# Kernel optimization log

Measured on AMD Instinct MI355X. Metric: run time of the kernel, lower is better.

Reference implementation:

```python
import jax, jax.numpy as jnp
import numpy as np

EMBED_DIM = 768
NUM_HEADS = 12
HEAD_DIM = EMBED_DIM // NUM_HEADS  # 64
SCALE = HEAD_DIM ** 0.5  # NOTE: source MULTIPLIES by sqrt(head_dim) (likely a bug, kept faithful)


def setup_inputs() -> dict:
    key = jax.random.key(0)
    kx, kq, kk, kv, ko = jax.random.split(key, 5)
    B, N, E = 8, 2048, EMBED_DIM
    s = 1.0 / np.sqrt(E)
    return {
        "x": jax.random.normal(kx, (B, N, E), dtype=jnp.float32),
        # nn.Linear weights stored [out_features, in_features], y = x @ W.T
        "Wq": jax.random.normal(kq, (E, E), dtype=jnp.float32) * s,
        "Wk": jax.random.normal(kk, (E, E), dtype=jnp.float32) * s,
        "Wv": jax.random.normal(kv, (E, E), dtype=jnp.float32) * s,
        "Wo": jax.random.normal(ko, (E, E), dtype=jnp.float32) * s,
    }


def reference(x, Wq, Wk, Wv, Wo):
    # Projections (no bias)
    q = jnp.einsum("bne,fe->bnf", x, Wq)
    k = jnp.einsum("bne,fe->bnf", x, Wk)
    v = jnp.einsum("bne,fe->bnf", x, Wv)
    # Full-width attention over the entire embedding dim (no head split, per source)
    energy = jnp.einsum("bid,bjd->bij", q, k) * SCALE  # [B, N, N]
    attn = jax.nn.softmax(energy, axis=-1)
    out = jnp.einsum("bij,bjd->bid", attn, v)  # [B, N, E]
    return jnp.einsum("bne,fe->bnf", out, Wo)
```

## Files before the change

### kernel.cpp

```cpp
#include <hip/hip_runtime.h>
#include <stdint.h>

typedef __bf16 bf16;
typedef __bf16 bf16x4 __attribute__((ext_vector_type(4)));
typedef __bf16 bf16x8 __attribute__((ext_vector_type(8)));
typedef float  f32x4  __attribute__((ext_vector_type(4)));

constexpr int BB = 8;
constexpr int NN = 2048;
constexpr int EE = 768;
constexpr int MM = BB * NN;
constexpr int E2 = 2 * EE;

typedef const __attribute__((address_space(1))) void* as1_cvp;
typedef __attribute__((address_space(3))) void* as3_vp;

static __device__ __forceinline__ void gld16(const void* g, void* l) {
  __builtin_amdgcn_global_load_lds((as1_cvp)g, (as3_vp)l, 16, 0, 0);
}

__global__ __launch_bounds__(256) void k_splitx(const float4* __restrict__ x,
                                                bf16x4* __restrict__ hi,
                                                bf16x4* __restrict__ lo, int n4) {
  int i = blockIdx.x * 256 + threadIdx.x;
  int st = gridDim.x * 256;
  for (; i < n4; i += st) {
    float4 v = x[i];
    bf16x4 h, l;
    h[0] = (bf16)v.x; l[0] = (bf16)(v.x - (float)h[0]);
    h[1] = (bf16)v.y; l[1] = (bf16)(v.y - (float)h[1]);
    h[2] = (bf16)v.z; l[2] = (bf16)(v.z - (float)h[2]);
    h[3] = (bf16)v.w; l[3] = (bf16)(v.w - (float)h[3]);
    hi[i] = h; lo[i] = l;
  }
}

__global__ __launch_bounds__(256) void k_wprep(const float4* __restrict__ wq,
                                               const float4* __restrict__ wk,
                                               const float4* __restrict__ wv,
                                               const float4* __restrict__ wo,
                                               bf16x4* __restrict__ qkh, bf16x4* __restrict__ qkl,
                                               bf16x4* __restrict__ vb,  bf16x4* __restrict__ ob) {
  const int n4 = EE * EE / 4;
  int sel = blockIdx.y;
  int i = blockIdx.x * 256 + threadIdx.x;
  int st = gridDim.x * 256;
  for (; i < n4; i += st) {
    if (sel <= 1) {
      float4 v = sel == 0 ? wq[i] : wk[i];
      bf16x4 h, l;
      h[0] = (bf16)v.x; l[0] = (bf16)(v.x - (float)h[0]);
      h[1] = (bf16)v.y; l[1] = (bf16)(v.y - (float)h[1]);
      h[2] = (bf16)v.z; l[2] = (bf16)(v.z - (float)h[2]);
      h[3] = (bf16)v.w; l[3] = (bf16)(v.w - (float)h[3]);
      int o = i + sel * n4;
      qkh[o] = h; qkl[o] = l;
    } else {
      float4 v = sel == 2 ? wv[i] : wo[i];
      bf16x4 h;
      h[0] = (bf16)v.x; h[1] = (bf16)v.y; h[2] = (bf16)v.z; h[3] = (bf16)v.w;
      if (sel == 2) vb[i] = h; else ob[i] = h;
    }
  }
}

template <bool SPLIT, int EPI>
__global__ __launch_bounds__(256, 2) void k_gemm(
    const bf16* __restrict__ Ah, const bf16* __restrict__ Al,
    const bf16* __restrict__ Bh, const bf16* __restrict__ Bl,
    void* __restrict__ C0, void* __restrict__ C1,
    int Kdim, int lda, int ldb, int ldc,
    long long sA, long long sB, long long sC, float cscale) {
  constexpr int NTILES = SPLIT ? 4 : 2;
  __shared__ __align__(16) bf16 sm[NTILES * 128 * 64];
  bf16* smAh = sm;
  bf16* smBh = sm + 128 * 64;
  bf16* smAl = SPLIT ? sm + 2 * 128 * 64 : nullptr;
  bf16* smBl = SPLIT ? sm + 3 * 128 * 64 : nullptr;

  const int tid = threadIdx.x;
  const int lane = tid & 63, wid = tid >> 6;
  const int lr = lane & 15, lq = lane >> 4;
  const int wr = (wid >> 1) * 64, wc = (wid & 1) * 64;
  const long long bz = blockIdx.z;
  const int col0 = blockIdx.x * 128, row0 = blockIdx.y * 128;

  const bf16* pAh = Ah + bz * sA;
  const bf16* pBh = Bh + bz * sB;
  const bf16* pAl = SPLIT ? (Al + bz * sA) : nullptr;
  const bf16* pBl = SPLIT ? (Bl + bz * sB) : nullptr;

  f32x4 acc[4][4] = {};

  for (int kt = 0; kt < Kdim; kt += 64) {
    {
      int o = tid * 16;
#pragma unroll
      for (int r = 0; r < 4; r++, o += 4096) {
        int row = o >> 7;
        int c = (o & 127) ^ ((row & 7) << 4);
        gld16((const char*)(pAh + (size_t)(row0 + row) * lda + kt) + c, (char*)smAh + o);
        gld16((const char*)(pBh + (size_t)(col0 + row) * ldb + kt) + c, (char*)smBh + o);
        if constexpr (SPLIT) {
          gld16((const char*)(pAl + (size_t)(row0 + row) * lda + kt) + c, (char*)smAl + o);
          gld16((const char*)(pBl + (size_t)(col0 + row) * ldb + kt) + c, (char*)smBl + o);
        }
      }
    }
    __syncthreads();
#pragma unroll
    for (int kk = 0; kk < 2; kk++) {
      bf16x8 ah[4], bh[4], al[4], bl[4];
#pragma unroll
      for (int i = 0; i < 4; i++) {
        int ar = wr + i * 16 + lr;
        int ao = ar * 128 + ((kk * 64 + lq * 16) ^ ((ar & 7) << 4));
        ah[i] = *(const bf16x8*)((const char*)smAh + ao);
        int br = wc + i * 16 + lr;
        int bo = br * 128 + ((kk * 64 + lq * 16) ^ ((br & 7) << 4));
        bh[i] = *(const bf16x8*)((const char*)smBh + bo);
        if constexpr (SPLIT) {
          al[i] = *(const bf16x8*)((const char*)smAl + ao);
          bl[i] = *(const bf16x8*)((const char*)smBl + bo);
        }
      }
#pragma unroll
      for (int i = 0; i < 4; i++)
#pragma unroll
        for (int j = 0; j < 4; j++) {
          acc[i][j] = __builtin_amdgcn_mfma_f32_16x16x32_bf16(ah[i], bh[j], acc[i][j], 0, 0, 0);
          if constexpr (SPLIT) {
            acc[i][j] = __builtin_amdgcn_mfma_f32_16x16x32_bf16(ah[i], bl[j], acc[i][j], 0, 0, 0);
            acc[i][j] = __builtin_amdgcn_mfma_f32_16x16x32_bf16(al[i], bh[j], acc[i][j], 0, 0, 0);
          }
        }
    }
    __syncthreads();
  }

#pragma unroll
  for (int i = 0; i < 4; i++) {
#pragma unroll
    for (int j2 = 0; j2 < 4; j2++) {
      f32x4 v = acc[i][j2];
      if constexpr (EPI == 3) {
        int r0 = row0 + wr + i * 16 + lq * 4;
        int c = col0 + wc + j2 * 16 + lr;
        int b = r0 >> 11, n0 = r0 & 2047;
        bf16x4 t;
#pragma unroll
        for (int j = 0; j < 4; j++) t[j] = (bf16)(v[j] * cscale);
        *(bf16x4*)((bf16*)C0 + ((size_t)b * EE + c) * NN + n0) = t;
      } else {
#pragma unroll
        for (int j = 0; j < 4; j++) {
          size_t r = (size_t)(row0 + wr + i * 16 + lq * 4 + j);
          size_t c = (size_t)(col0 + wc + j2 * 16 + lr);
          size_t idx = r * (size_t)ldc + c;
          float val = v[j] * cscale;
          if constexpr (EPI == 0) {
            bf16* Chp = (bf16*)C0 + bz * sC;
            bf16* Clp = (bf16*)C1 + bz * sC;
            bf16 h = (bf16)val;
            Chp[idx] = h;
            Clp[idx] = (bf16)(val - (float)h);
          } else if constexpr (EPI == 1) {
            float* Cp = (float*)C0 + bz * sC;
            Cp[idx] = val;
          } else {
            bf16* Cp = (bf16*)C0 + bz * sC;
            Cp[idx] = (bf16)val;
          }
        }
      }
    }
  }
}

__global__ __launch_bounds__(256) void k_softmax(float* __restrict__ S) {
  size_t row = blockIdx.x;
  float* srow = S + row * (size_t)NN;
  int tid = threadIdx.x;
  int wid = tid >> 6, lane = tid & 63;
  const float4* s4 = (const float4*)srow;
  float4 v0 = s4[tid * 2], v1 = s4[tid * 2 + 1];
  float vv[8] = {v0.x, v0.y, v0.z, v0.w, v1.x, v1.y, v1.z, v1.w};
  float m = vv[0];
#pragma unroll
  for (int j = 1; j < 8; j++) m = fmaxf(m, vv[j]);
#pragma unroll
  for (int d = 1; d < 64; d <<= 1) m = fmaxf(m, __shfl_xor(m, d));
  __shared__ float red[8];
  if (lane == 0) red[wid] = m;
  __syncthreads();
  m = fmaxf(fmaxf(red[0], red[1]), fmaxf(red[2], red[3]));
  float e[8];
  float ssum = 0.f;
#pragma unroll
  for (int j = 0; j < 8; j++) { e[j] = __expf(vv[j] - m); ssum += e[j]; }
#pragma unroll
  for (int d = 1; d < 64; d <<= 1) ssum += __shfl_xor(ssum, d);
  if (lane == 0) red[4 + wid] = ssum;
  __syncthreads();
  ssum = red[4] + red[5] + red[6] + red[7];
  float inv = 1.0f / ssum;
  bf16x8 p;
#pragma unroll
  for (int j = 0; j < 8; j++) p[j] = (bf16)(e[j] * inv);
  *(bf16x8*)((bf16*)srow + tid * 8) = p;
}

extern "C" void kernel_launch(void* const* d_in, const int* in_sizes, int n_in,
                              void* d_out, int out_size, void* d_ws, size_t ws_size,
                              hipStream_t stream) {
  const float* x  = (const float*)d_in[0];
  const float* Wq = (const float*)d_in[1];
  const float* Wk = (const float*)d_in[2];
  const float* Wv = (const float*)d_in[3];
  const float* Wo = (const float*)d_in[4];
  float* out = (float*)d_out;
  char* ws = (char*)d_ws;

  const size_t szXE = (size_t)MM * EE * 2;
  const size_t szWb = (size_t)EE * EE * 2;
  const size_t szQKh = (size_t)MM * E2 * 2;
  const size_t szS1 = (size_t)NN * NN * 4;

  bf16* xhi = (bf16*)(ws);
  bf16* xlo = (bf16*)(ws + szXE);
  char* wb  = ws + 2 * szXE;
  bf16* wqkh = (bf16*)(wb);
  bf16* wqkl = (bf16*)(wb + 2 * szWb);
  bf16* wvb  = (bf16*)(wb + 4 * szWb);
  bf16* wob  = (bf16*)(wb + 5 * szWb);
  char* qkb = wb + 6 * szWb;
  bf16* QKh = (bf16*)(qkb);
  bf16* QKl = (bf16*)(qkb + szQKh);
  bf16* Vt  = (bf16*)(qkb + 2 * szQKh);
  char* Sb  = qkb + 2 * szQKh + szXE;
  float* S  = (float*)Sb;
  bf16* Ao  = (bf16*)ws;

  size_t oS = (size_t)(Sb - ws);
  size_t avail = ws_size > oS ? ws_size - oS : 0;
  int G = 8;
  while (G > 1 && (size_t)G * szS1 > avail) G >>= 1;

  k_splitx<<<2048, 256, 0, stream>>>((const float4*)x, (bf16x4*)xhi, (bf16x4*)xlo, MM * EE / 4);
  k_wprep<<<dim3(144, 4), 256, 0, stream>>>((const float4*)Wq, (const float4*)Wk,
                                            (const float4*)Wv, (const float4*)Wo,
                                            (bf16x4*)wqkh, (bf16x4*)wqkl, (bf16x4*)wvb, (bf16x4*)wob);

  k_gemm<true, 0><<<dim3(E2 / 128, MM / 128, 1), 256, 0, stream>>>(
      xhi, xlo, wqkh, wqkl, QKh, QKl, EE, EE, EE, E2, 0, 0, 0, 1.0f);
  k_gemm<false, 3><<<dim3(EE / 128, MM / 128, 1), 256, 0, stream>>>(
      xhi, nullptr, wvb, nullptr, Vt, nullptr, EE, EE, EE, 0, 0, 0, 0, 1.0f);

  const long long sQK = (long long)NN * E2;
  for (int g = 0; g < BB; g += G) {
    const bf16* Qh = QKh + (size_t)g * NN * E2;
    const bf16* Ql = QKl + (size_t)g * NN * E2;
    k_gemm<true, 1><<<dim3(NN / 128, NN / 128, G), 256, 0, stream>>>(
        Qh, Ql, Qh + EE, Ql + EE, S, nullptr, EE, E2, E2, NN,
        sQK, sQK, (long long)NN * NN, 8.0f);
    k_softmax<<<G * NN, 256, 0, stream>>>(S);
    k_gemm<false, 2><<<dim3(EE / 128, NN / 128, G), 256, 0, stream>>>(
        (const bf16*)S, nullptr, Vt + (size_t)g * EE * NN, nullptr,
        Ao + (size_t)g * NN * EE, nullptr, NN, 2 * NN, NN, EE,
        2LL * NN * NN, (long long)EE * NN, (long long)NN * EE, 1.0f);
  }

  k_gemm<false, 1><<<dim3(EE / 128, MM / 128, 1), 256, 0, stream>>>(
      Ao, nullptr, wob, nullptr, out, nullptr, EE, EE, EE, EE, 0, 0, 0, 1.0f);
}
```

Baseline: 448.8 us.

## Add triple-buffered 256x128 split-bf16 GEMM kernel for QK projection and energy

Adds a new 512-thread kernel for the split-precision (hi/lo bf16) GEMMs, used for the QK projection and the Q·K^T energy product. It uses 256x128 output tiles, a triple-buffered LDS ring filled by direct global-to-LDS loads with an XOR swizzle, and explicit vmcnt waits and barriers to overlap loads with MFMA. It also remaps blocks across XCDs and raises wave priority around the MFMA bursts. The goal is to hide memory latency and increase reuse in the dominant GEMMs. The cost is about 144KB of LDS per block, which limits occupancy to one block per CU, plus hand-tuned synchronisation that is fragile.

```diff
diff --git a/kernel.cpp b/kernel.cpp
--- a/kernel.cpp
+++ b/kernel.cpp
@@ -64,6 +64,144 @@
   }
 }
 
+template <int EPI>
+__global__ __launch_bounds__(512, 2) void k_gemm_split8(
+    const bf16* __restrict__ Ah, const bf16* __restrict__ Al,
+    const bf16* __restrict__ Bh, const bf16* __restrict__ Bl,
+    void* __restrict__ C0, void* __restrict__ C1,
+    int Kdim, int lda, int ldb, int ldc,
+    long long sA, long long sB, long long sC, float cscale) {
+  __shared__ __align__(16) char sm[3 * 49152];
+
+  const int tid = threadIdx.x;
+  const int lane = tid & 63, wid = tid >> 6;
+  const int lr = lane & 15, lq = lane >> 4;
+  const int wm = wid >> 1, wn = wid & 1;
+
+  const int nbx = gridDim.x;
+  int lin = blockIdx.x + blockIdx.y * nbx;
+  int chunk = (nbx * gridDim.y) >> 3;
+  int sw = (lin & 7) * chunk + (lin >> 3);
+  const int col0 = (sw % nbx) * 128;
+  const int row0 = (sw / nbx) * 256;
+  const long long bz = blockIdx.z;
+
+  const bf16* pAh = Ah + bz * sA + (size_t)row0 * lda;
+  const bf16* pAl = Al + bz * sA + (size_t)row0 * lda;
+  const bf16* pBh = Bh + bz * sB + (size_t)col0 * ldb;
+  const bf16* pBl = Bl + bz * sB + (size_t)col0 * ldb;
+
+  int aoff[4], boff[4];
+#pragma unroll
+  for (int m = 0; m < 4; ++m) {
+    int row = wm * 64 + m * 16 + lr;
+    int o = row * 64 + lq * 16;
+    aoff[m] = o ^ (((o >> 7) & 3) << 4);
+  }
+#pragma unroll
+  for (int n = 0; n < 4; ++n) {
+    int row = wn * 64 + n * 16 + lr;
+    int o = row * 64 + lq * 16;
+    boff[n] = o ^ (((o >> 7) & 3) << 4);
+  }
+
+  const int o0 = tid * 16;
+  auto stage_half = [&](int buf, int tk, bool hi) {
+    char* base = sm + buf * 49152;
+    const bf16* a = hi ? pAh : pAl;
+    const bf16* b = hi ? pBh : pBl;
+    char* da = base + (hi ? 0 : 16384);
+    char* db = base + (hi ? 32768 : 40960);
+#pragma unroll
+    for (int r = 0; r < 2; ++r) {
+      int o = o0 + r * 8192;
+      int row = o >> 6;
+      int cb = (o & 63) ^ (((o >> 7) & 3) << 4);
+      gld16((const char*)(a + (size_t)row * lda) + tk * 64 + cb, da + o);
+    }
+    {
+      int row = o0 >> 6;
+      int cb = (o0 & 63) ^ (((o0 >> 7) & 3) << 4);
+      gld16((const char*)(b + (size_t)row * ldb) + tk * 64 + cb, db + o0);
+    }
+  };
+
+  f32x4 acc[4][4] = {};
+  const int NT = Kdim >> 5;
+
+  stage_half(0, 0, true);  stage_half(0, 0, false);
+  stage_half(1, 1, true);  stage_half(1, 1, false);
+  asm volatile("s_waitcnt vmcnt(6)" ::: "memory");
+  __builtin_amdgcn_s_barrier();
+
+  bf16x8 bhf[4], blf[4];
+  for (int j = 0; j < NT; ++j) {
+    const char* bb = sm + (j % 3) * 49152;
+    const int nb = (j + 2) % 3;
+    const bool pf = (j + 2) < NT;
+#pragma unroll
+    for (int h = 0; h < 2; ++h) {
+      if (pf) stage_half(nb, j + 2, h == 0);
+      bf16x8 ah[2], al[2];
+      if (h == 0) {
+#pragma unroll
+        for (int n = 0; n < 4; ++n) {
+          bhf[n] = *(const bf16x8*)(bb + 32768 + boff[n]);
+          blf[n] = *(const bf16x8*)(bb + 40960 + boff[n]);
+        }
+      }
+#pragma unroll
+      for (int mm = 0; mm < 2; ++mm) {
+        ah[mm] = *(const bf16x8*)(bb + aoff[h * 2 + mm]);
+        al[mm] = *(const bf16x8*)(bb + 16384 + aoff[h * 2 + mm]);
+      }
+      if (h == 1) {
+        if (j < NT - 2)       asm volatile("s_waitcnt vmcnt(6)" ::: "memory");
+        else if (j == NT - 2) asm volatile("s_waitcnt vmcnt(0)" ::: "memory");
+      }
+      __builtin_amdgcn_s_barrier();
+      asm volatile("s_waitcnt lgkmcnt(0)" ::: "memory");
+      __builtin_amdgcn_sched_barrier(0);
+      __builtin_amdgcn_s_setprio(1);
+#pragma unroll
+      for (int mm = 0; mm < 2; ++mm)
+#pragma unroll
+        for (int n = 0; n < 4; ++n) {
+          acc[h * 2 + mm][n] = __builtin_amdgcn_mfma_f32_16x16x32_bf16(ah[mm], bhf[n], acc[h * 2 + mm][n], 0, 0, 0);
+          acc[h * 2 + mm][n] = __builtin_amdgcn_mfma_f32_16x16x32_bf16(ah[mm], blf[n], acc[h * 2 + mm][n], 0, 0, 0);
+          acc[h * 2 + mm][n] = __builtin_amdgcn_mfma_f32_16x16x32_bf16(al[mm], bhf[n], acc[h * 2 + mm][n], 0, 0, 0);
+        }
+      __builtin_amdgcn_s_setprio(0);
+      __builtin_amdgcn_s_barrier();
+    }
+  }
+
+#pragma unroll
+  for (int m = 0; m < 4; ++m) {
+#pragma unroll
+    for (int n = 0; n < 4; ++n) {
+      f32x4 v = acc[m][n];
+#pragma unroll
+      for (int jj = 0; jj < 4; ++jj) {
+        size_t r = (size_t)(row0 + wm * 64 + m * 16 + lq * 4 + jj);
+        size_t c = (size_t)(col0 + wn * 64 + n * 16 + lr);
+        size_t idx = r * (size_t)ldc + c;
+        float val = v[jj] * cscale;
+        if constexpr (EPI == 0) {
+          bf16* Chp = (bf16*)C0 + bz * sC;
+          bf16* Clp = (bf16*)C1 + bz * sC;
+          bf16 hh = (bf16)val;
+          Chp[idx] = hh;
+          Clp[idx] = (bf16)(val - (float)hh);
+        } else {
+          float* Cp = (float*)C0 + bz * sC;
+          Cp[idx] = val;
+        }
+      }
+    }
+  }
+}
+
 template <bool SPLIT, int EPI>
 __global__ __launch_bounds__(256, 2) void k_gemm(
     const bf16* __restrict__ Ah, const bf16* __restrict__ Al,
@@ -72,11 +210,11 @@
     int Kdim, int lda, int ldb, int ldc,
     long long sA, long long sB, long long sC, float cscale) {
   constexpr int NTILES = SPLIT ? 4 : 2;
-  __shared__ __align__(16) bf16 sm[NTILES * 128 * 64];
-  bf16* smAh = sm;
-  bf16* smBh = sm + 128 * 64;
-  bf16* smAl = SPLIT ? sm + 2 * 128 * 64 : nullptr;
-  bf16* smBl = SPLIT ? sm + 3 * 128 * 64 : nullptr;
+  __shared__ __align__(16) bf16 smm[NTILES * 128 * 64];
+  bf16* smAh = smm;
+  bf16* smBh = smm + 128 * 64;
+  bf16* smAl = SPLIT ? smm + 2 * 128 * 64 : nullptr;
+  bf16* smBl = SPLIT ? smm + 3 * 128 * 64 : nullptr;
 
   const int tid = threadIdx.x;
   const int lane = tid & 63, wid = tid >> 6;
@@ -158,13 +296,7 @@
           size_t c = (size_t)(col0 + wc + j2 * 16 + lr);
           size_t idx = r * (size_t)ldc + c;
           float val = v[j] * cscale;
-          if constexpr (EPI == 0) {
-            bf16* Chp = (bf16*)C0 + bz * sC;
-            bf16* Clp = (bf16*)C1 + bz * sC;
-            bf16 h = (bf16)val;
-            Chp[idx] = h;
-            Clp[idx] = (bf16)(val - (float)h);
-          } else if constexpr (EPI == 1) {
+          if constexpr (EPI == 1) {
             float* Cp = (float*)C0 + bz * sC;
             Cp[idx] = val;
           } else {
@@ -251,7 +383,7 @@
                                             (const float4*)Wv, (const float4*)Wo,
                                             (bf16x4*)wqkh, (bf16x4*)wqkl, (bf16x4*)wvb, (bf16x4*)wob);
 
-  k_gemm<true, 0><<<dim3(E2 / 128, MM / 128, 1), 256, 0, stream>>>(
+  k_gemm_split8<0><<<dim3(E2 / 128, MM / 256, 1), 512, 0, stream>>>(
       xhi, xlo, wqkh, wqkl, QKh, QKl, EE, EE, EE, E2, 0, 0, 0, 1.0f);
   k_gemm<false, 3><<<dim3(EE / 128, MM / 128, 1), 256, 0, stream>>>(
       xhi, nullptr, wvb, nullptr, Vt, nullptr, EE, EE, EE, 0, 0, 0, 0, 1.0f);
@@ -260,7 +392,7 @@
   for (int g = 0; g < BB; g += G) {
     const bf16* Qh = QKh + (size_t)g * NN * E2;
     const bf16* Ql = QKl + (size_t)g * NN * E2;
-    k_gemm<true, 1><<<dim3(NN / 128, NN / 128, G), 256, 0, stream>>>(
+    k_gemm_split8<1><<<dim3(NN / 128, NN / 256, G), 512, 0, stream>>>(
         Qh, Ql, Qh + EE, Ql + EE, S, nullptr, EE, E2, E2, NN,
         sQK, sQK, (long long)NN * NN, 8.0f);
     k_softmax<<<G * NN, 256, 0, stream>>>(S);
```

Result: slower. 482.7 us (+7.5%).

## Add 256x256 tiled split-bf16 GEMM kernel for QK projection and scores

Applied to the files above, without the earlier changes.

Adds a new GEMM kernel with 512 threads and 256x256 output tiles. It treats the three split-precision products (hi*hi, hi*lo, lo*hi) as one concatenated K loop of 36 steps, replacing the old per-k-tile split handling. The kernel uses XOR-swizzled LDS loaded through global_load_lds, double buffering with staggered A/B prefetch, s_setprio around the MFMAs, and a blockwise grid swizzle for L2 locality. It is used for the fused Q/K projection and the QK^T score GEMM, where it should raise arithmetic intensity and overlap loads with MFMAs. The cost is 128KB of LDS per block, which limits occupancy, plus heavier register pressure from the 8x4 accumulator tile.

```diff
diff --git a/kernel.cpp b/kernel.cpp
--- a/kernel.cpp
+++ b/kernel.cpp
@@ -64,6 +64,133 @@
   }
 }
 
+template <int EPI>
+__global__ __launch_bounds__(512, 2) void k_gemm3p8(
+    const bf16* __restrict__ A0, const bf16* __restrict__ A1, const bf16* __restrict__ A2,
+    const bf16* __restrict__ B0, const bf16* __restrict__ B1, const bf16* __restrict__ B2,
+    void* __restrict__ C0, void* __restrict__ C1,
+    int lda, int ldb, int ldc,
+    long long sA, long long sB, long long sC, float cscale) {
+  constexpr int NT = 36;
+  __shared__ __align__(16) char sm[131072];
+
+  const int tid = threadIdx.x;
+  const int lane = tid & 63, wid = tid >> 6;
+  const int lr = lane & 15, lq = lane >> 4;
+  const int wm = wid >> 2, wn = wid & 3;
+
+  const int nbx = gridDim.x;
+  int lin = blockIdx.x + blockIdx.y * nbx;
+  int chunk = (nbx * gridDim.y) >> 3;
+  int sw = (lin & 7) * chunk + (lin >> 3);
+  const int col0 = (sw % nbx) * 256;
+  const int row0 = (sw / nbx) * 256;
+  const long long bz = blockIdx.z;
+
+  const bf16* pA[3] = {A0 + bz * sA, A1 + bz * sA, A2 + bz * sA};
+  const bf16* pB[3] = {B0 + bz * sB, B1 + bz * sB, B2 + bz * sB};
+
+  auto stage = [&](int tensor, int half, int tk, int buf) {
+    int pi = tk / 12;
+    int ko = (tk - pi * 12) * 64;
+    const bf16* base;
+    if (tensor == 0) base = pi == 0 ? pA[0] : (pi == 1 ? pA[1] : pA[2]);
+    else             base = pi == 0 ? pB[0] : (pi == 1 ? pB[1] : pB[2]);
+    int ld = tensor == 0 ? lda : ldb;
+    int rt0 = tensor == 0 ? row0 : col0;
+    char* dst = sm + tensor * 65536 + buf * 32768 + half * 16384;
+#pragma unroll
+    for (int r = 0; r < 2; ++r) {
+      int o = tid * 16 + r * 8192;
+      int row = half * 128 + (o >> 7);
+      int cc = (o >> 4) & 7;
+      int c = cc ^ (row & 7);
+      gld16((const char*)(base + (size_t)(rt0 + row) * ld + ko) + c * 16, dst + o);
+    }
+  };
+
+  const int c0 = ((0 + lq) ^ (lr & 7)) * 16;
+  const int c1 = ((4 + lq) ^ (lr & 7)) * 16;
+
+  f32x4 acc[8][4] = {};
+  bf16x8 bf[4][2];
+
+  stage(0, 0, 0, 0); stage(0, 1, 0, 0); stage(1, 0, 0, 0); stage(1, 1, 0, 0);
+  stage(1, 0, 1, 1); stage(1, 1, 1, 1);
+  asm volatile("s_waitcnt vmcnt(4)" ::: "memory");
+  __builtin_amdgcn_s_barrier();
+  __builtin_amdgcn_sched_barrier(0);
+
+  for (int T = 0; T < NT; ++T) {
+    const int buf = T & 1;
+    const int a_lds = buf * 32768 + (wm * 128 + lr) * 128;
+    const int b_lds = 65536 + buf * 32768 + (wn * 64 + lr) * 128;
+#pragma unroll
+    for (int p = 0; p < 4; ++p) {
+      if (p == 0) { if (T + 1 < NT) stage(0, 0, T + 1, buf ^ 1); }
+      if (p == 1) { if (T + 1 < NT) stage(0, 1, T + 1, buf ^ 1); }
+      if (p == 2) { if (T + 2 < NT) stage(1, 0, T + 2, buf); }
+      if (p == 3) { if (T + 2 < NT) stage(1, 1, T + 2, buf); }
+      if (p == 0) {
+#pragma unroll
+        for (int ni = 0; ni < 4; ++ni) {
+          bf[ni][0] = *(const bf16x8*)(sm + b_lds + ni * 2048 + c0);
+          bf[ni][1] = *(const bf16x8*)(sm + b_lds + ni * 2048 + c1);
+        }
+      }
+      bf16x8 af[2][2];
+#pragma unroll
+      for (int m2 = 0; m2 < 2; ++m2) {
+        af[m2][0] = *(const bf16x8*)(sm + a_lds + (2 * p + m2) * 2048 + c0);
+        af[m2][1] = *(const bf16x8*)(sm + a_lds + (2 * p + m2) * 2048 + c1);
+      }
+      asm volatile("s_waitcnt lgkmcnt(0)" ::: "memory");
+      __builtin_amdgcn_sched_barrier(0);
+      __builtin_amdgcn_s_setprio(1);
+#pragma unroll
+      for (int kk = 0; kk < 2; ++kk)
+#pragma unroll
+        for (int m2 = 0; m2 < 2; ++m2)
+#pragma unroll
+          for (int ni = 0; ni < 4; ++ni)
+            acc[2 * p + m2][ni] = __builtin_amdgcn_mfma_f32_16x16x32_bf16(
+                af[m2][kk], bf[ni][kk], acc[2 * p + m2][ni], 0, 0, 0);
+      __builtin_amdgcn_s_setprio(0);
+      if (p == 3) {
+        if (T < NT - 2) asm volatile("s_waitcnt vmcnt(4)" ::: "memory");
+        else            asm volatile("s_waitcnt vmcnt(0)" ::: "memory");
+      }
+      __builtin_amdgcn_s_barrier();
+      __builtin_amdgcn_sched_barrier(0);
+    }
+  }
+
+#pragma unroll
+  for (int mi = 0; mi < 8; ++mi) {
+#pragma unroll
+    for (int ni = 0; ni < 4; ++ni) {
+      f32x4 v = acc[mi][ni];
+#pragma unroll
+      for (int jj = 0; jj < 4; ++jj) {
+        size_t r = (size_t)(row0 + wm * 128 + mi * 16 + lq * 4 + jj);
+        size_t c = (size_t)(col0 + wn * 64 + ni * 16 + lr);
+        size_t idx = r * (size_t)ldc + c;
+        float val = v[jj] * cscale;
+        if constexpr (EPI == 0) {
+          bf16* Chp = (bf16*)C0 + bz * sC;
+          bf16* Clp = (bf16*)C1 + bz * sC;
+          bf16 hh = (bf16)val;
+          Chp[idx] = hh;
+          Clp[idx] = (bf16)(val - (float)hh);
+        } else {
+          float* Cp = (float*)C0 + bz * sC;
+          Cp[idx] = val;
+        }
+      }
+    }
+  }
+}
+
 template <bool SPLIT, int EPI>
 __global__ __launch_bounds__(256, 2) void k_gemm(
     const bf16* __restrict__ Ah, const bf16* __restrict__ Al,
@@ -72,11 +199,11 @@
     int Kdim, int lda, int ldb, int ldc,
     long long sA, long long sB, long long sC, float cscale) {
   constexpr int NTILES = SPLIT ? 4 : 2;
-  __shared__ __align__(16) bf16 sm[NTILES * 128 * 64];
-  bf16* smAh = sm;
-  bf16* smBh = sm + 128 * 64;
-  bf16* smAl = SPLIT ? sm + 2 * 128 * 64 : nullptr;
-  bf16* smBl = SPLIT ? sm + 3 * 128 * 64 : nullptr;
+  __shared__ __align__(16) bf16 smm[NTILES * 128 * 64];
+  bf16* smAh = smm;
+  bf16* smBh = smm + 128 * 64;
+  bf16* smAl = SPLIT ? smm + 2 * 128 * 64 : nullptr;
+  bf16* smBl = SPLIT ? smm + 3 * 128 * 64 : nullptr;
 
   const int tid = threadIdx.x;
   const int lane = tid & 63, wid = tid >> 6;
@@ -158,13 +285,7 @@
           size_t c = (size_t)(col0 + wc + j2 * 16 + lr);
           size_t idx = r * (size_t)ldc + c;
           float val = v[j] * cscale;
-          if constexpr (EPI == 0) {
-            bf16* Chp = (bf16*)C0 + bz * sC;
-            bf16* Clp = (bf16*)C1 + bz * sC;
-            bf16 h = (bf16)val;
-            Chp[idx] = h;
-            Clp[idx] = (bf16)(val - (float)h);
-          } else if constexpr (EPI == 1) {
+          if constexpr (EPI == 1) {
             float* Cp = (float*)C0 + bz * sC;
             Cp[idx] = val;
           } else {
@@ -251,8 +372,8 @@
                                             (const float4*)Wv, (const float4*)Wo,
                                             (bf16x4*)wqkh, (bf16x4*)wqkl, (bf16x4*)wvb, (bf16x4*)wob);
 
-  k_gemm<true, 0><<<dim3(E2 / 128, MM / 128, 1), 256, 0, stream>>>(
-      xhi, xlo, wqkh, wqkl, QKh, QKl, EE, EE, EE, E2, 0, 0, 0, 1.0f);
+  k_gemm3p8<0><<<dim3(E2 / 256, MM / 256, 1), 512, 0, stream>>>(
+      xhi, xhi, xlo, wqkh, wqkl, wqkh, QKh, QKl, EE, EE, E2, 0, 0, 0, 1.0f);
   k_gemm<false, 3><<<dim3(EE / 128, MM / 128, 1), 256, 0, stream>>>(
       xhi, nullptr, wvb, nullptr, Vt, nullptr, EE, EE, EE, 0, 0, 0, 0, 1.0f);
 
@@ -260,8 +381,8 @@
   for (int g = 0; g < BB; g += G) {
     const bf16* Qh = QKh + (size_t)g * NN * E2;
     const bf16* Ql = QKl + (size_t)g * NN * E2;
-    k_gemm<true, 1><<<dim3(NN / 128, NN / 128, G), 256, 0, stream>>>(
-        Qh, Ql, Qh + EE, Ql + EE, S, nullptr, EE, E2, E2, NN,
+    k_gemm3p8<1><<<dim3(NN / 256, NN / 256, G), 512, 0, stream>>>(
+        Qh, Qh, Ql, Qh + EE, Ql + EE, Qh + EE, S, nullptr, E2, E2, NN,
         sQK, sQK, (long long)NN * NN, 8.0f);
     k_softmax<<<G * NN, 256, 0, stream>>>(S);
     k_gemm<false, 2><<<dim3(EE / 128, NN / 128, G), 256, 0, stream>>>(
```

New measurement: 481.0 us. 7.2% more time.

## Fuse softmax statistics into QK GEMM epilogue and apply exp inside PV GEMM

Applied to the files above, without the earlier changes.

Removes the standalone softmax pass. The QK^T GEMM epilogue now writes per-row partial (max, sum-exp) values for each 64-column chunk. A small combine kernel reduces these into a row max and an inverse sum. A new PV kernel then reads the raw fp32 scores, applies exp and normalisation on the fly, converts to bf16 into LDS and runs the MFMA GEMM. This saves a full read-and-write pass over the score matrix. In exchange the PV kernel reads fp32 instead of bf16 scores, redoes the exponentials for every output column block, and loads A synchronously rather than through async global-to-LDS copies.

```diff
diff --git a/kernel.cpp b/kernel.cpp
--- a/kernel.cpp
+++ b/kernel.cpp
@@ -1,5 +1,6 @@
 #include <hip/hip_runtime.h>
 #include <stdint.h>
+#include <math.h>
 
 typedef __bf16 bf16;
 typedef __bf16 bf16x4 __attribute__((ext_vector_type(4)));
@@ -70,13 +71,14 @@
     const bf16* __restrict__ Bh, const bf16* __restrict__ Bl,
     void* __restrict__ C0, void* __restrict__ C1,
     int Kdim, int lda, int ldb, int ldc,
-    long long sA, long long sB, long long sC, float cscale) {
+    long long sA, long long sB, long long sC, float cscale,
+    float2* __restrict__ part) {
   constexpr int NTILES = SPLIT ? 4 : 2;
-  __shared__ __align__(16) bf16 sm[NTILES * 128 * 64];
-  bf16* smAh = sm;
-  bf16* smBh = sm + 128 * 64;
-  bf16* smAl = SPLIT ? sm + 2 * 128 * 64 : nullptr;
-  bf16* smBl = SPLIT ? sm + 3 * 128 * 64 : nullptr;
+  __shared__ __align__(16) bf16 smm[NTILES * 128 * 64];
+  bf16* smAh = smm;
+  bf16* smBh = smm + 128 * 64;
+  bf16* smAl = SPLIT ? smm + 2 * 128 * 64 : nullptr;
+  bf16* smBl = SPLIT ? smm + 3 * 128 * 64 : nullptr;
 
   const int tid = threadIdx.x;
   const int lane = tid & 63, wid = tid >> 6;
@@ -164,7 +166,7 @@
             bf16 h = (bf16)val;
             Chp[idx] = h;
             Clp[idx] = (bf16)(val - (float)h);
-          } else if constexpr (EPI == 1) {
+          } else if constexpr (EPI == 1 || EPI == 4) {
             float* Cp = (float*)C0 + bz * sC;
             Cp[idx] = val;
           } else {
@@ -175,39 +177,137 @@
       }
     }
   }
-}
-
-__global__ __launch_bounds__(256) void k_softmax(float* __restrict__ S) {
-  size_t row = blockIdx.x;
-  float* srow = S + row * (size_t)NN;
-  int tid = threadIdx.x;
-  int wid = tid >> 6, lane = tid & 63;
-  const float4* s4 = (const float4*)srow;
-  float4 v0 = s4[tid * 2], v1 = s4[tid * 2 + 1];
-  float vv[8] = {v0.x, v0.y, v0.z, v0.w, v1.x, v1.y, v1.z, v1.w};
-  float m = vv[0];
-#pragma unroll
-  for (int j = 1; j < 8; j++) m = fmaxf(m, vv[j]);
-#pragma unroll
-  for (int d = 1; d < 64; d <<= 1) m = fmaxf(m, __shfl_xor(m, d));
-  __shared__ float red[8];
-  if (lane == 0) red[wid] = m;
-  __syncthreads();
-  m = fmaxf(fmaxf(red[0], red[1]), fmaxf(red[2], red[3]));
-  float e[8];
-  float ssum = 0.f;
-#pragma unroll
-  for (int j = 0; j < 8; j++) { e[j] = __expf(vv[j] - m); ssum += e[j]; }
-#pragma unroll
-  for (int d = 1; d < 64; d <<= 1) ssum += __shfl_xor(ssum, d);
-  if (lane == 0) red[4 + wid] = ssum;
-  __syncthreads();
-  ssum = red[4] + red[5] + red[6] + red[7];
-  float inv = 1.0f / ssum;
-  bf16x8 p;
-#pragma unroll
-  for (int j = 0; j < 8; j++) p[j] = (bf16)(e[j] * inv);
-  *(bf16x8*)((bf16*)srow + tid * 8) = p;
+
+  if constexpr (EPI == 4) {
+    float2* pp = part + bz * ((long long)NN * 32);
+    const int entry = (col0 + wc) >> 6;
+#pragma unroll
+    for (int i = 0; i < 4; i++) {
+#pragma unroll
+      for (int j = 0; j < 4; j++) {
+        float m = acc[i][0][j];
+#pragma unroll
+        for (int j2 = 1; j2 < 4; j2++) m = fmaxf(m, acc[i][j2][j]);
+        m *= cscale;
+#pragma unroll
+        for (int d = 1; d < 16; d <<= 1) m = fmaxf(m, __shfl_xor(m, d));
+        float s = 0.f;
+#pragma unroll
+        for (int j2 = 0; j2 < 4; j2++) s += __expf(acc[i][j2][j] * cscale - m);
+#pragma unroll
+        for (int d = 1; d < 16; d <<= 1) s += __shfl_xor(s, d);
+        if (lr == 0) {
+          int row = row0 + wr + i * 16 + lq * 4 + j;
+          float2 t; t.x = m; t.y = s;
+          pp[(size_t)row * 32 + entry] = t;
+        }
+      }
+    }
+  }
+}
+
+__global__ __launch_bounds__(256) void k_combine(const float2* __restrict__ part,
+                                                 float2* __restrict__ rs) {
+  int row = blockIdx.x * 256 + threadIdx.x;
+  const float2* p = part + (size_t)row * 32;
+  float M = p[0].x;
+#pragma unroll
+  for (int e = 1; e < 32; e++) M = fmaxf(M, p[e].x);
+  float S = 0.f;
+#pragma unroll
+  for (int e = 0; e < 32; e++) S += p[e].y * __expf(p[e].x - M);
+  float2 t; t.x = M; t.y = 1.0f / S;
+  rs[row] = t;
+}
+
+__global__ __launch_bounds__(256, 3) void k_pv(const float* __restrict__ S,
+                                               const float2* __restrict__ rs,
+                                               const bf16* __restrict__ Vt,
+                                               bf16* __restrict__ Ao) {
+  __shared__ __align__(16) bf16 smA[128 * 64];
+  __shared__ __align__(16) bf16 smB[128 * 64];
+
+  const int tid = threadIdx.x;
+  const int lane = tid & 63, wid = tid >> 6;
+  const int lr = lane & 15, lq = lane >> 4;
+  const int wr = (wid >> 1) * 64, wc = (wid & 1) * 64;
+  const long long bz = blockIdx.z;
+  const int col0 = blockIdx.x * 128, row0 = blockIdx.y * 128;
+
+  const float* pS = S + bz * (long long)NN * NN;
+  const bf16*  pB = Vt + bz * (long long)EE * NN;
+
+  const int arow = tid >> 1;
+  const int ach = tid & 1;
+  const float2 mr = rs[bz * NN + row0 + arow];
+  const float* srcrow = pS + (size_t)(row0 + arow) * NN + ach * 32;
+
+  f32x4 acc[4][4] = {};
+
+  for (int kt = 0; kt < NN; kt += 64) {
+    const float4* src = (const float4*)(srcrow + kt);
+    float4 f[8];
+#pragma unroll
+    for (int q = 0; q < 8; q++) f[q] = src[q];
+#pragma unroll
+    for (int q2 = 0; q2 < 4; q2++) {
+      float4 a0 = f[2 * q2], a1 = f[2 * q2 + 1];
+      bf16x8 pk;
+      pk[0] = (bf16)(__expf(a0.x - mr.x) * mr.y);
+      pk[1] = (bf16)(__expf(a0.y - mr.x) * mr.y);
+      pk[2] = (bf16)(__expf(a0.z - mr.x) * mr.y);
+      pk[3] = (bf16)(__expf(a0.w - mr.x) * mr.y);
+      pk[4] = (bf16)(__expf(a1.x - mr.x) * mr.y);
+      pk[5] = (bf16)(__expf(a1.y - mr.x) * mr.y);
+      pk[6] = (bf16)(__expf(a1.z - mr.x) * mr.y);
+      pk[7] = (bf16)(__expf(a1.w - mr.x) * mr.y);
+      int cb = ach * 4 + q2;
+      *(bf16x8*)((char*)smA + arow * 128 + ((cb ^ (arow & 7)) << 4)) = pk;
+    }
+    {
+      int o = tid * 16;
+#pragma unroll
+      for (int r = 0; r < 4; r++, o += 4096) {
+        int row = o >> 7;
+        int c = (o & 127) ^ ((row & 7) << 4);
+        gld16((const char*)(pB + (size_t)(col0 + row) * NN + kt) + c, (char*)smB + o);
+      }
+    }
+    __syncthreads();
+#pragma unroll
+    for (int kk = 0; kk < 2; kk++) {
+      bf16x8 ah[4], bh[4];
+#pragma unroll
+      for (int i = 0; i < 4; i++) {
+        int ar = wr + i * 16 + lr;
+        int ao = ar * 128 + ((kk * 64 + lq * 16) ^ ((ar & 7) << 4));
+        ah[i] = *(const bf16x8*)((const char*)smA + ao);
+        int br = wc + i * 16 + lr;
+        int bo = br * 128 + ((kk * 64 + lq * 16) ^ ((br & 7) << 4));
+        bh[i] = *(const bf16x8*)((const char*)smB + bo);
+      }
+#pragma unroll
+      for (int i = 0; i < 4; i++)
+#pragma unroll
+        for (int j = 0; j < 4; j++)
+          acc[i][j] = __builtin_amdgcn_mfma_f32_16x16x32_bf16(ah[i], bh[j], acc[i][j], 0, 0, 0);
+    }
+    __syncthreads();
+  }
+
+#pragma unroll
+  for (int i = 0; i < 4; i++) {
+#pragma unroll
+    for (int j2 = 0; j2 < 4; j2++) {
+      f32x4 v = acc[i][j2];
+#pragma unroll
+      for (int j = 0; j < 4; j++) {
+        size_t r = (size_t)(row0 + wr + i * 16 + lq * 4 + j);
+        size_t c = (size_t)(col0 + wc + j2 * 16 + lr);
+        Ao[bz * (long long)NN * EE + r * EE + c] = (bf16)v[j];
+      }
+    }
+  }
 }
 
 extern "C" void kernel_launch(void* const* d_in, const int* in_sizes, int n_in,
@@ -240,6 +340,8 @@
   char* Sb  = qkb + 2 * szQKh + szXE;
   float* S  = (float*)Sb;
   bf16* Ao  = (bf16*)ws;
+  float2* part = (float2*)(ws + szXE);
+  float2* rs   = (float2*)(ws + szXE + (size_t)BB * NN * 32 * sizeof(float2));
 
   size_t oS = (size_t)(Sb - ws);
   size_t avail = ws_size > oS ? ws_size - oS : 0;
@@ -252,24 +354,22 @@
                                             (bf16x4*)wqkh, (bf16x4*)wqkl, (bf16x4*)wvb, (bf16x4*)wob);
 
   k_gemm<true, 0><<<dim3(E2 / 128, MM / 128, 1), 256, 0, stream>>>(
-      xhi, xlo, wqkh, wqkl, QKh, QKl, EE, EE, EE, E2, 0, 0, 0, 1.0f);
+      xhi, xlo, wqkh, wqkl, QKh, QKl, EE, EE, EE, E2, 0, 0, 0, 1.0f, nullptr);
   k_gemm<false, 3><<<dim3(EE / 128, MM / 128, 1), 256, 0, stream>>>(
-      xhi, nullptr, wvb, nullptr, Vt, nullptr, EE, EE, EE, 0, 0, 0, 0, 1.0f);
+      xhi, nullptr, wvb, nullptr, Vt, nullptr, EE, EE, EE, 0, 0, 0, 0, 1.0f, nullptr);
 
   const long long sQK = (long long)NN * E2;
   for (int g = 0; g < BB; g += G) {
     const bf16* Qh = QKh + (size_t)g * NN * E2;
     const bf16* Ql = QKl + (size_t)g * NN * E2;
-    k_gemm<true, 1><<<dim3(NN / 128, NN / 128, G), 256, 0, stream>>>(
+    k_gemm<true, 4><<<dim3(NN / 128, NN / 128, G), 256, 0, stream>>>(
         Qh, Ql, Qh + EE, Ql + EE, S, nullptr, EE, E2, E2, NN,
-        sQK, sQK, (long long)NN * NN, 8.0f);
-    k_softmax<<<G * NN, 256, 0, stream>>>(S);
-    k_gemm<false, 2><<<dim3(EE / 128, NN / 128, G), 256, 0, stream>>>(
-        (const bf16*)S, nullptr, Vt + (size_t)g * EE * NN, nullptr,
-        Ao + (size_t)g * NN * EE, nullptr, NN, 2 * NN, NN, EE,
-        2LL * NN * NN, (long long)EE * NN, (long long)NN * EE, 1.0f);
+        sQK, sQK, (long long)NN * NN, 8.0f, part);
+    k_combine<<<G * NN / 256, 256, 0, stream>>>(part, rs);
+    k_pv<<<dim3(EE / 128, NN / 128, G), 256, 0, stream>>>(
+        S, rs, Vt + (size_t)g * EE * NN, Ao + (size_t)g * NN * EE);
   }
 
   k_gemm<false, 1><<<dim3(EE / 128, MM / 128, 1), 256, 0, stream>>>(
-      Ao, nullptr, wob, nullptr, out, nullptr, EE, EE, EE, EE, 0, 0, 0, 1.0f);
-}
+      Ao, nullptr, wob, nullptr, out, nullptr, EE, EE, EE, EE, 0, 0, 0, 1.0f, nullptr);
+}
```

Measured after the change: 577.2 us. 1.29x slower.
